# Kernel tuning notes

Measured on AMD Instinct MI355X. Metric: run time of the kernel, lower is better.

## Reference

```python
import jax, jax.numpy as jnp
import numpy as np

B, T, D, S, K = 8, 4096, 1024, 64, 3
EPS = 1e-5

def setup_inputs() -> dict:
    key = jax.random.key(0)
    ks = jax.random.split(key, 10)
    def lin(k, out_d, in_d):
        s = 1.0 / np.sqrt(in_d)
        return jax.random.uniform(k, (out_d, in_d), jnp.float32, -s, s)
    return {
        "x": jax.random.normal(ks[0], (B, T, D), jnp.float32),
        "norm_w": jnp.ones((D,), jnp.float32),
        "norm_b": jnp.zeros((D,), jnp.float32),
        "in_w": lin(ks[1], 2 * D, D),
        "in_b": jnp.zeros((2 * D,), jnp.float32),
        "conv_w": jax.random.normal(ks[2], (D, 1, K), jnp.float32) / np.sqrt(K),
        "conv_b": jnp.zeros((D,), jnp.float32),
        "dt_w": lin(ks[3], S, D),
        "dt_b": jnp.zeros((S,), jnp.float32),
        "b_w": lin(ks[4], S, D),
        "b_b": jnp.zeros((S,), jnp.float32),
        "c_w": lin(ks[5], S, D),
        "c_b": jnp.zeros((S,), jnp.float32),
        "a_log": jax.random.normal(ks[6], (S,), jnp.float32) * 0.02,
        "d": jnp.ones((D,), jnp.float32),
        "out_w": lin(ks[7], D, D + S),
        "out_b": jnp.zeros((D,), jnp.float32),
    }

def reference(x, norm_w, norm_b, in_w, in_b, conv_w, conv_b,
              dt_w, dt_b, b_w, b_b, c_w, c_b, a_log, d, out_w, out_b):
    bsz, tlen, dim = x.shape
    sdim = a_log.shape[0]
    k = conv_w.shape[-1]
    residual = x
    # LayerNorm
    mu = jnp.mean(x, axis=-1, keepdims=True)
    var = jnp.mean(jnp.square(x - mu), axis=-1, keepdims=True)
    xn = (x - mu) * jax.lax.rsqrt(var + EPS) * norm_w + norm_b
    # in_proj and chunk
    h = xn @ in_w.T + in_b                       # (B,T,2D)
    x_proj, z = jnp.split(h, 2, axis=-1)         # each (B,T,D)
    # depthwise conv over time, 'same' padding
    xc = jax.lax.conv_general_dilated(
        x_proj.transpose(0, 2, 1), conv_w, (1,), [(k // 2, k // 2)],
        dimension_numbers=("NCH", "OIH", "NCH"), feature_group_count=dim)
    x_conv = jnp.tanh((xc + conv_b[None, :, None]).transpose(0, 2, 1))  # (B,T,D)
    # gate projections for all timesteps at once
    dt = jax.nn.softplus(z @ dt_w.T + dt_b) + 1e-4   # (B,T,S)
    b = jnp.tanh(z @ b_w.T + b_b)                    # (B,T,S)
    c = jnp.tanh(z @ c_w.T + c_b)                    # (B,T,S)
    a = -jnp.exp(a_log)                              # (S,)
    decay = jnp.exp(a * dt)                          # (B,T,S)
    # linear recurrence: state_t = state_{t-1} * decay_t + b_t
    def step(state, inp):
        dec_t, b_t = inp
        state = state * dec_t + b_t
        return state, state
    _, states = jax.lax.scan(step, jnp.zeros((bsz, sdim), x.dtype),
                             (decay.transpose(1, 0, 2), b.transpose(1, 0, 2)))
    states = states.transpose(1, 0, 2)               # (B,T,S)
    y = c * states
    mix = jnp.concatenate([x_conv * d, y], axis=-1)  # (B,T,D+S)
    out = mix @ out_w.T + out_b                      # (B,T,D)
    return residual + out
```

## Files before the change

kernel.cpp:

```cpp
#include <hip/hip_runtime.h>

#define TT 4096
#define DD 1024
#define NN 32768

typedef short s16x8 __attribute__((ext_vector_type(8)));
typedef float f32x4 __attribute__((ext_vector_type(4)));
typedef unsigned short ushort_t;

__device__ __forceinline__ unsigned short f2bf(float f) {
  unsigned u = __float_as_uint(f);
  u += 0x7FFFu + ((u >> 16) & 1u);
  return (unsigned short)(u >> 16);
}
__device__ __forceinline__ float bf2f(unsigned short h) {
  return __uint_as_float(((unsigned)h) << 16);
}
__device__ __forceinline__ void load_lds16(const void* g, void* l) {
  __builtin_amdgcn_global_load_lds(
      (const __attribute__((address_space(1))) unsigned int*)g,
      (__attribute__((address_space(3))) unsigned int*)l, 16, 0, 0);
}

__global__ __launch_bounds__(256)
void cvt_kernel(const float* __restrict__ s, ushort_t* __restrict__ d, int n) {
  int i = (blockIdx.x * 256 + threadIdx.x) * 4;
  if (i < n) {
    float4 v = *(const float4*)&s[i];
    ushort4 o; o.x = f2bf(v.x); o.y = f2bf(v.y); o.z = f2bf(v.z); o.w = f2bf(v.w);
    *(ushort4*)&d[i] = o;
  }
}

__global__ __launch_bounds__(256)
void w3pad_kernel(const float* __restrict__ dt_w, const float* __restrict__ b_w,
                  const float* __restrict__ c_w, ushort_t* __restrict__ w3) {
  int e = (blockIdx.x * 256 + threadIdx.x) * 4;
  int row = e >> 10, col = e & 1023;
  float4 v; v.x = 0.f; v.y = 0.f; v.z = 0.f; v.w = 0.f;
  if (row < 64)       v = *(const float4*)&dt_w[(row << 10) + col];
  else if (row < 128) v = *(const float4*)&b_w[((row - 64) << 10) + col];
  else if (row < 192) v = *(const float4*)&c_w[((row - 128) << 10) + col];
  ushort4 o; o.x = f2bf(v.x); o.y = f2bf(v.y); o.z = f2bf(v.z); o.w = f2bf(v.w);
  *(ushort4*)&w3[e] = o;
}

__global__ __launch_bounds__(256)
void tpose_kernel(const float* __restrict__ src, ushort_t* __restrict__ dst) {
  __shared__ float tile[64][65];
  int bx = blockIdx.x & 15, by = blockIdx.x >> 4;
  int tx = threadIdx.x & 63, ty0 = threadIdx.x >> 6;
  #pragma unroll
  for (int i = 0; i < 16; ++i) {
    int ty = ty0 * 16 + i;
    tile[ty][tx] = src[(size_t)(by * 64 + ty) * 1024 + bx * 64 + tx];
  }
  __syncthreads();
  #pragma unroll
  for (int i = 0; i < 16; ++i) {
    int ty = ty0 * 16 + i;
    dst[(size_t)(bx * 64 + ty) * 1024 + by * 64 + tx] = f2bf(tile[tx][ty]);
  }
}

__global__ void gbias_kernel(const float* __restrict__ dt_w, const float* __restrict__ b_w,
                             const float* __restrict__ c_w, const float* __restrict__ dt_b,
                             const float* __restrict__ b_b, const float* __restrict__ c_b,
                             const float* __restrict__ in_b, float* __restrict__ gb) {
  int i = blockIdx.x, lane = threadIdx.x;
  const float* wr = i < 64 ? dt_w + (size_t)i * 1024
                  : i < 128 ? b_w + (size_t)(i - 64) * 1024
                            : c_w + (size_t)(i - 128) * 1024;
  float s = 0.f;
  for (int j = lane; j < 1024; j += 64) s += wr[j] * in_b[1024 + j];
  #pragma unroll
  for (int off = 32; off; off >>= 1) s += __shfl_xor(s, off, 64);
  if (lane == 0) {
    float bb = i < 64 ? dt_b[i] : i < 128 ? b_b[i - 64] : c_b[i - 128];
    gb[i] = s + bb;
  }
}

__global__ __launch_bounds__(256)
void ln_kernel(const float* __restrict__ x, const float* __restrict__ w,
               const float* __restrict__ bv, ushort_t* __restrict__ xn)
{
  int row = blockIdx.x * 4 + (threadIdx.x >> 6);
  int lane = threadIdx.x & 63;
  const float* xr = x + (size_t)row * DD;
  float4 v[4];
  float s = 0.f, ss = 0.f;
  #pragma unroll
  for (int j = 0; j < 4; ++j) {
    v[j] = *(const float4*)&xr[j * 256 + lane * 4];
    s  += v[j].x + v[j].y + v[j].z + v[j].w;
    ss += v[j].x * v[j].x + v[j].y * v[j].y + v[j].z * v[j].z + v[j].w * v[j].w;
  }
  #pragma unroll
  for (int off = 32; off > 0; off >>= 1) {
    s  += __shfl_xor(s, off, 64);
    ss += __shfl_xor(ss, off, 64);
  }
  float mean = s * (1.f / 1024.f);
  float var  = ss * (1.f / 1024.f) - mean * mean;
  float rinv = rsqrtf(var + 1e-5f);
  #pragma unroll
  for (int j = 0; j < 4; ++j) {
    int c = j * 256 + lane * 4;
    float4 wv = *(const float4*)&w[c];
    float4 bb = *(const float4*)&bv[c];
    ushort4 o;
    o.x = f2bf((v[j].x - mean) * rinv * wv.x + bb.x);
    o.y = f2bf((v[j].y - mean) * rinv * wv.y + bb.y);
    o.z = f2bf((v[j].z - mean) * rinv * wv.z + bb.z);
    o.w = f2bf((v[j].w - mean) * rinv * wv.w + bb.w);
    *(ushort4*)&xn[(size_t)row * DD + c] = o;
  }
}

template<int EP>
__global__ __launch_bounds__(512, 2)
void gemm256(const ushort_t* __restrict__ A, const ushort_t* __restrict__ W,
             int M, int N, int K,
             const float* __restrict__ bias0,
             ushort_t* __restrict__ o0, ushort_t* __restrict__ o1)
{
  __shared__ ushort_t lds[65536];
  const int tid = threadIdx.x;
  const int lane = tid & 63;
  const int wid = tid >> 6;
  const int wr = wid >> 2;
  const int wc = wid & 3;
  const int lane15 = lane & 15;
  const int lgrp = lane >> 4;
  const int rsw = (lane15 & 7) << 4;
  const int ntn = N >> 8;
  int bid = blockIdx.x;
  { const int cpx = (int)gridDim.x >> 3; bid = (bid & 7) * cpx + (bid >> 3); }
  const int brow = (bid / ntn) << 8;
  const int bcol = (bid % ntn) << 8;
  const int nk = K >> 6;
  const int sRow = tid >> 3;
  const int sCol = (tid & 7) << 4;
  const char* ldsb = (const char*)lds;
  (void)M;

#define STG(bufb, isB, h, kt) do { \
    const int ktc_ = (kt) < nk ? (kt) : nk - 1; \
    const ushort_t* gsrc_ = (isB) ? W : A; \
    const int rowb_ = ((isB) ? bcol : brow) + (h) * 128; \
    _Pragma("unroll") \
    for (int j_ = 0; j_ < 2; ++j_) { \
      const int r_ = j_ * 64 + sRow; \
      load_lds16((const char*)(gsrc_ + (size_t)(rowb_ + r_) * K) + ktc_ * 128 + (sCol ^ ((r_ & 7) << 4)), \
                 (char*)lds + (bufb) * 65536 + (isB) * 32768 + (h) * 16384 + r_ * 128 + sCol); \
    } } while (0)

#define LDA_(bufb, m, kk) \
  (*(const s16x8*)(ldsb + (bufb) * 65536 + wr * 16384 + ((m) * 16 + lane15) * 128 + (((kk) * 64 + lgrp * 16) ^ rsw)))
#define LDB_(bufb, n, kk) \
  (*(const s16x8*)(ldsb + (bufb) * 65536 + 32768 + (wc >> 1) * 16384 + ((wc & 1) * 64 + (n) * 16 + lane15) * 128 + (((kk) * 64 + lgrp * 16) ^ rsw)))

#define BARR() asm volatile("s_barrier" ::: "memory")
#define VMW2() asm volatile("s_waitcnt vmcnt(2)" ::: "memory")
#define VMW4() asm volatile("s_waitcnt vmcnt(4)" ::: "memory")

#define RDA(dst, bufb, mh) do { \
    _Pragma("unroll") for (int kk = 0; kk < 2; ++kk) \
    _Pragma("unroll") for (int q = 0; q < 4; ++q) \
      dst[kk][q] = LDA_(bufb, (mh) * 4 + q, kk); } while (0)
#define RDB(dst, bufb, nh) do { \
    _Pragma("unroll") for (int kk = 0; kk < 2; ++kk) \
    _Pragma("unroll") for (int p = 0; p < 2; ++p) \
      dst[kk][p] = LDB_(bufb, (nh) * 2 + p, kk); } while (0)

#define MFMAQ(AF, BF, mh, nh) do { \
    __builtin_amdgcn_s_setprio(1); \
    _Pragma("unroll") for (int kk = 0; kk < 2; ++kk) \
    _Pragma("unroll") for (int q = 0; q < 4; ++q) \
    _Pragma("unroll") for (int p = 0; p < 2; ++p) \
      acc[(mh) * 4 + q][(nh) * 2 + p] = __builtin_amdgcn_mfma_f32_16x16x32_bf16( \
          AF[kk][q], BF[kk][p], acc[(mh) * 4 + q][(nh) * 2 + p], 0, 0, 0); \
    __builtin_amdgcn_s_setprio(0); } while (0)

  f32x4 acc[8][4];
  #pragma unroll
  for (int m = 0; m < 8; ++m) {
    #pragma unroll
    for (int n = 0; n < 4; ++n) acc[m][n] = (f32x4){0.f, 0.f, 0.f, 0.f};
  }
  s16x8 afP[2][4], afQ[2][4];
  s16x8 b0[2][2], b1[2][2];

  STG(0, 1, 0, 0); STG(0, 0, 0, 0); STG(0, 0, 1, 0); STG(0, 1, 1, 0);
  STG(1, 1, 0, 1); STG(1, 0, 0, 1);
  VMW4(); BARR();
  RDA(afP, 0, 0); RDB(b0, 0, 0);

  const int nIter = nk >> 1;
  for (int it = 0; it < nIter; ++it) {
    const int t0 = 2 * it;
    STG(1, 0, 1, t0 + 1);
    MFMAQ(afP, b0, 0, 0);
    RDB(b1, 0, 1); BARR();
    STG(1, 1, 1, t0 + 1);
    MFMAQ(afP, b1, 0, 1);
    RDA(afQ, 0, 1); BARR();
    STG(0, 1, 0, t0 + 2);
    MFMAQ(afQ, b1, 1, 1);
    VMW2(); BARR();
    STG(0, 0, 0, t0 + 2);
    MFMAQ(afQ, b0, 1, 0);
    RDA(afP, 1, 0); RDB(b1, 1, 1); BARR();
    STG(0, 0, 1, t0 + 2);
    MFMAQ(afP, b1, 0, 1);
    RDB(b0, 1, 0); BARR();
    STG(0, 1, 1, t0 + 2);
    MFMAQ(afP, b0, 0, 0);
    RDA(afQ, 1, 1); BARR();
    STG(1, 1, 0, t0 + 3);
    MFMAQ(afQ, b0, 1, 0);
    VMW2(); BARR();
    STG(1, 0, 0, t0 + 3);
    MFMAQ(afQ, b1, 1, 1);
    RDA(afP, 0, 0); RDB(b0, 0, 0); BARR();
  }
  if (nk & 1) {
    MFMAQ(afP, b0, 0, 0);
    RDB(b1, 0, 1);
    MFMAQ(afP, b1, 0, 1);
    RDA(afQ, 0, 1);
    MFMAQ(afQ, b1, 1, 1);
    MFMAQ(afQ, b0, 1, 0);
  }

#undef STG
#undef LDA_
#undef LDB_
#undef BARR
#undef VMW2
#undef VMW4
#undef RDA
#undef RDB
#undef MFMAQ

  #pragma unroll
  for (int m = 0; m < 8; ++m) {
    #pragma unroll
    for (int i = 0; i < 4; ++i) {
      const int r = brow + wr * 128 + m * 16 + lgrp * 4 + i;
      #pragma unroll
      for (int n = 0; n < 4; ++n) {
        const int col = bcol + wc * 64 + n * 16 + lane15;
        float v = acc[m][n][i] + bias0[col];
        if (col < DD) o0[(size_t)r * DD + col] = f2bf(v);
        else          o1[(size_t)r * DD + (col - DD)] = f2bf(v);
      }
    }
  }
}

__global__ __launch_bounds__(256, 2)
void gemm3_128(const ushort_t* __restrict__ A, const ushort_t* __restrict__ W,
               int M, int N, int K,
               const float* __restrict__ bias, const float* __restrict__ resid,
               float* __restrict__ outf)
{
  __shared__ ushort_t lds[32768];
  const int tid = threadIdx.x;
  const int lane = tid & 63;
  const int wid = tid >> 6;
  const int wr = wid >> 1;
  const int wc = wid & 1;
  const int lane15 = lane & 15;
  const int lgrp = lane >> 4;
  const int rsw = (lane15 & 7) << 4;
  const int ntn = N >> 7;
  int bid = blockIdx.x;
  { const int cpx = (int)gridDim.x >> 3; bid = (bid & 7) * cpx + (bid >> 3); }
  const int brow = (bid / ntn) << 7;
  const int bcol = (bid % ntn) << 7;
  const int nk = K >> 6;
  const int sRow = tid >> 3;
  const int sCol = (tid & 7) << 4;
  const char* ldsb = (const char*)lds;
  (void)M;

  f32x4 acc[4][4];
  #pragma unroll
  for (int q = 0; q < 4; ++q)
    #pragma unroll
    for (int p = 0; p < 4; ++p) acc[q][p] = (f32x4){0.f, 0.f, 0.f, 0.f};

#define STG3(bufb, kt) do { \
    _Pragma("unroll") \
    for (int j_ = 0; j_ < 4; ++j_) { \
      const int r_ = j_ * 32 + sRow; \
      load_lds16((const char*)(A + (size_t)(brow + r_) * K) + (kt) * 128 + (sCol ^ ((r_ & 7) << 4)), \
                 (char*)lds + (bufb) * 32768 + r_ * 128 + sCol); \
      load_lds16((const char*)(W + (size_t)(bcol + r_) * K) + (kt) * 128 + (sCol ^ ((r_ & 7) << 4)), \
                 (char*)lds + (bufb) * 32768 + 16384 + r_ * 128 + sCol); \
    } } while (0)
#define BARR3() asm volatile("s_barrier" ::: "memory")
#define VMW8() asm volatile("s_waitcnt vmcnt(8)" ::: "memory")
#define VMW0() asm volatile("s_waitcnt vmcnt(0)" ::: "memory")

  STG3(0, 0);

  for (int t = 0; t < nk; ++t) {
    const int cur = t & 1;
    if (t + 1 < nk) { STG3(cur ^ 1, t + 1); VMW8(); }
    else            { VMW0(); }
    BARR3();
    #pragma unroll
    for (int kk = 0; kk < 2; ++kk) {
      s16x8 af[4], bf[4];
      #pragma unroll
      for (int q = 0; q < 4; ++q)
        af[q] = *(const s16x8*)(ldsb + cur * 32768 +
                 (wr * 64 + q * 16 + lane15) * 128 + ((kk * 64 + lgrp * 16) ^ rsw));
      #pragma unroll
      for (int p = 0; p < 4; ++p)
        bf[p] = *(const s16x8*)(ldsb + cur * 32768 + 16384 +
                 (wc * 64 + p * 16 + lane15) * 128 + ((kk * 64 + lgrp * 16) ^ rsw));
      __builtin_amdgcn_s_setprio(1);
      #pragma unroll
      for (int q = 0; q < 4; ++q)
        #pragma unroll
        for (int p = 0; p < 4; ++p)
          acc[q][p] = __builtin_amdgcn_mfma_f32_16x16x32_bf16(af[q], bf[p], acc[q][p], 0, 0, 0);
      __builtin_amdgcn_s_setprio(0);
    }
    BARR3();
  }
#undef STG3
#undef BARR3
#undef VMW8
#undef VMW0

  #pragma unroll
  for (int q = 0; q < 4; ++q) {
    #pragma unroll
    for (int i = 0; i < 4; ++i) {
      const int r = brow + wr * 64 + q * 16 + lgrp * 4 + i;
      #pragma unroll
      for (int p = 0; p < 4; ++p) {
        const int col = bcol + wc * 64 + p * 16 + lane15;
        outf[(size_t)r * DD + col] = acc[q][p][i] + bias[col] + resid[(size_t)r * DD + col];
      }
    }
  }
}

__global__ __launch_bounds__(256)
void gemm128w(const ushort_t* __restrict__ A, const ushort_t* __restrict__ W,
              int M, int N, int K, ushort_t* __restrict__ o0)
{
  __shared__ ushort_t As[128 * 64];
  __shared__ ushort_t Bs[128 * 64];
  const int tid = threadIdx.x;
  const int lane = tid & 63;
  const int wid = tid >> 6;
  const int ntn = N >> 7;
  const int brow = (blockIdx.x / ntn) << 7;
  const int bcol = (blockIdx.x % ntn) << 7;
  const int wr = (wid >> 1) << 6;
  const int wc = (wid & 1) << 6;
  const int lane15 = lane & 15;
  const int lgrp = lane >> 4;
  (void)M;

  f32x4 acc[4][4];
  #pragma unroll
  for (int m = 0; m < 4; ++m)
    #pragma unroll
    for (int n = 0; n < 4; ++n)
      acc[m][n] = (f32x4){0.f, 0.f, 0.f, 0.f};

  const int r0 = tid >> 3;
  const int c0 = (tid & 7) << 3;
  const ushort_t* gA = A + (size_t)(brow + r0) * K + c0;
  const ushort_t* gW = W + (size_t)(bcol + r0) * K + c0;
  ushort_t* lA = &As[r0 * 64 + c0];
  ushort_t* lB = &Bs[r0 * 64 + c0];

  for (int k0 = 0; k0 < K; k0 += 64) {
    #pragma unroll
    for (int j = 0; j < 4; ++j) {
      load_lds16(gA + (size_t)(j * 32) * K + k0, lA + j * 32 * 64);
      load_lds16(gW + (size_t)(j * 32) * K + k0, lB + j * 32 * 64);
    }
    __syncthreads();
    #pragma unroll
    for (int kk = 0; kk < 2; ++kk) {
      s16x8 af[4], bfr[4];
      #pragma unroll
      for (int m = 0; m < 4; ++m)
        af[m] = *(const s16x8*)&As[(wr + m * 16 + lane15) * 64 + kk * 32 + lgrp * 8];
      #pragma unroll
      for (int n = 0; n < 4; ++n)
        bfr[n] = *(const s16x8*)&Bs[(wc + n * 16 + lane15) * 64 + kk * 32 + lgrp * 8];
      #pragma unroll
      for (int m = 0; m < 4; ++m)
        #pragma unroll
        for (int n = 0; n < 4; ++n)
          acc[m][n] = __builtin_amdgcn_mfma_f32_16x16x32_bf16(af[m], bfr[n], acc[m][n], 0, 0, 0);
    }
    __syncthreads();
  }

  #pragma unroll
  for (int m = 0; m < 4; ++m) {
    #pragma unroll
    for (int i = 0; i < 4; ++i) {
      const int r = brow + wr + m * 16 + lgrp * 4 + i;
      #pragma unroll
      for (int n = 0; n < 4; ++n) {
        const int col = bcol + wc + n * 16 + lane15;
        o0[(size_t)r * N + col] = f2bf(acc[m][n][i]);
      }
    }
  }
}

__global__ __launch_bounds__(256)
void gemm128g(const ushort_t* __restrict__ A, const ushort_t* __restrict__ W,
              int M, int N, int K,
              const float* __restrict__ gb, const float* __restrict__ alog,
              float* __restrict__ g0, float* __restrict__ g1, float* __restrict__ g2)
{
  __shared__ ushort_t As[128 * 64];
  __shared__ ushort_t Bs[128 * 64];
  const int tid = threadIdx.x;
  const int lane = tid & 63;
  const int wid = tid >> 6;
  const int ntn = N >> 7;
  const int brow = (blockIdx.x / ntn) << 7;
  const int bcol = (blockIdx.x % ntn) << 7;
  const int wr = (wid >> 1) << 6;
  const int wc = (wid & 1) << 6;
  const int lane15 = lane & 15;
  const int lgrp = lane >> 4;
  (void)M;

  f32x4 acc[4][4];
  #pragma unroll
  for (int m = 0; m < 4; ++m)
    #pragma unroll
    for (int n = 0; n < 4; ++n)
      acc[m][n] = (f32x4){0.f, 0.f, 0.f, 0.f};

  const int r0 = tid >> 3;
  const int c0 = (tid & 7) << 3;
  const ushort_t* gA = A + (size_t)(brow + r0) * K + c0;
  const ushort_t* gW = W + (size_t)(bcol + r0) * K + c0;
  ushort_t* lA = &As[r0 * 64 + c0];
  ushort_t* lB = &Bs[r0 * 64 + c0];

  for (int k0 = 0; k0 < K; k0 += 64) {
    #pragma unroll
    for (int j = 0; j < 4; ++j) {
      load_lds16(gA + (size_t)(j * 32) * K + k0, lA + j * 32 * 64);
      load_lds16(gW + (size_t)(j * 32) * K + k0, lB + j * 32 * 64);
    }
    __syncthreads();
    #pragma unroll
    for (int kk = 0; kk < 2; ++kk) {
      s16x8 af[4], bfr[4];
      #pragma unroll
      for (int m = 0; m < 4; ++m)
        af[m] = *(const s16x8*)&As[(wr + m * 16 + lane15) * 64 + kk * 32 + lgrp * 8];
      #pragma unroll
      for (int n = 0; n < 4; ++n)
        bfr[n] = *(const s16x8*)&Bs[(wc + n * 16 + lane15) * 64 + kk * 32 + lgrp * 8];
      #pragma unroll
      for (int m = 0; m < 4; ++m)
        #pragma unroll
        for (int n = 0; n < 4; ++n)
          acc[m][n] = __builtin_amdgcn_mfma_f32_16x16x32_bf16(af[m], bfr[n], acc[m][n], 0, 0, 0);
    }
    __syncthreads();
  }

  #pragma unroll
  for (int m = 0; m < 4; ++m) {
    #pragma unroll
    for (int i = 0; i < 4; ++i) {
      const int r = brow + wr + m * 16 + lgrp * 4 + i;
      #pragma unroll
      for (int n = 0; n < 4; ++n) {
        const int col = bcol + wc + n * 16 + lane15;
        float v = acc[m][n][i];
        if (col < 64) {
          float u = v + gb[col];
          float sp = (u > 20.f) ? u : log1pf(expf(u));
          g0[(size_t)r * 64 + col] = expf(-expf(alog[col]) * (sp + 1e-4f));
        } else if (col < 128) {
          g1[(size_t)r * 64 + (col - 64)] = tanhf(v + gb[col]);
        } else if (col < 192) {
          g2[(size_t)r * 64 + (col - 128)] = tanhf(v + gb[col]);
        }
      }
    }
  }
}

__global__ __launch_bounds__(256)
void conv_kernel(const ushort_t* __restrict__ xp, const float* __restrict__ cw,
                 const float* __restrict__ cb, const float* __restrict__ dvec,
                 ushort_t* __restrict__ mix)
{
  int idx = blockIdx.x * 256 + threadIdx.x;
  int row = idx >> 7;
  int d0 = (idx & 127) << 3;
  int t = row & (TT - 1);
  s16x8 cur = *(const s16x8*)&xp[(size_t)row * DD + d0];
  s16x8 prv; s16x8 nxt;
  #pragma unroll
  for (int j = 0; j < 8; ++j) { prv[j] = 0; nxt[j] = 0; }
  if (t > 0)      prv = *(const s16x8*)&xp[(size_t)(row - 1) * DD + d0];
  if (t < TT - 1) nxt = *(const s16x8*)&xp[(size_t)(row + 1) * DD + d0];
  float wv[24];
  #pragma unroll
  for (int j = 0; j < 6; ++j) *(float4*)&wv[j * 4] = *(const float4*)&cw[d0 * 3 + j * 4];
  float cbv[8], dv[8];
  *(float4*)&cbv[0] = *(const float4*)&cb[d0];
  *(float4*)&cbv[4] = *(const float4*)&cb[d0 + 4];
  *(float4*)&dv[0]  = *(const float4*)&dvec[d0];
  *(float4*)&dv[4]  = *(const float4*)&dvec[d0 + 4];
  s16x8 o;
  #pragma unroll
  for (int j = 0; j < 8; ++j) {
    float acc = cbv[j] + bf2f((ushort_t)prv[j]) * wv[j * 3]
              + bf2f((ushort_t)cur[j]) * wv[j * 3 + 1]
              + bf2f((ushort_t)nxt[j]) * wv[j * 3 + 2];
    o[j] = (short)f2bf(tanhf(acc) * dv[j]);
  }
  *(s16x8*)&mix[(size_t)row * 1088 + d0] = o;
}

__global__ void scanA_kernel(const float* __restrict__ dec, const float* __restrict__ bb,
                             float* __restrict__ P, float* __restrict__ Q)
{
  int b = blockIdx.x >> 6, ci = blockIdx.x & 63, s = threadIdx.x;
  size_t base = (((size_t)b * TT) + ci * 64) * 64 + s;
  float p = 1.f, q = 0.f;
  #pragma unroll 4
  for (int t = 0; t < 64; ++t) {
    float d = dec[base + (size_t)t * 64];
    float w = bb[base + (size_t)t * 64];
    q = q * d + w; p *= d;
  }
  int o = (b * 64 + ci) * 64 + s;
  P[o] = p; Q[o] = q;
}

__global__ void scanB_kernel(const float* __restrict__ P, const float* __restrict__ Q,
                             float* __restrict__ I)
{
  int b = blockIdx.x, s = threadIdx.x;
  float pv[64], qv[64];
  #pragma unroll
  for (int ci = 0; ci < 64; ++ci) {
    int o = (b * 64 + ci) * 64 + s;
    pv[ci] = P[o]; qv[ci] = Q[o];
  }
  float st = 0.f;
  #pragma unroll
  for (int ci = 0; ci < 64; ++ci) {
    int o = (b * 64 + ci) * 64 + s;
    I[o] = st;
    st = st * pv[ci] + qv[ci];
  }
}

__global__ void scanC_kernel(const float* __restrict__ dec, const float* __restrict__ bb,
                             const float* __restrict__ cc, const float* __restrict__ I,
                             ushort_t* __restrict__ mix)
{
  int b = blockIdx.x >> 6, ci = blockIdx.x & 63, s = threadIdx.x;
  size_t base = (((size_t)b * TT) + ci * 64) * 64 + s;
  float st = I[(b * 64 + ci) * 64 + s];
  size_t mrow = (size_t)b * TT + ci * 64;
  #pragma unroll 4
  for (int t = 0; t < 64; ++t) {
    size_t o = base + (size_t)t * 64;
    st = st * dec[o] + bb[o];
    mix[(mrow + t) * 1088 + 1024 + s] = (ushort_t)f2bf(cc[o] * st);
  }
}

extern "C" void kernel_launch(void* const* d_in, const int* in_sizes, int n_in,
                              void* d_out, int out_size, void* d_ws, size_t ws_size,
                              hipStream_t stream)
{
  (void)in_sizes; (void)n_in; (void)out_size; (void)ws_size;
  const float* x      = (const float*)d_in[0];
  const float* norm_w = (const float*)d_in[1];
  const float* norm_b = (const float*)d_in[2];
  const float* in_w   = (const float*)d_in[3];
  const float* in_b   = (const float*)d_in[4];
  const float* conv_w = (const float*)d_in[5];
  const float* conv_b = (const float*)d_in[6];
  const float* dt_w   = (const float*)d_in[7];
  const float* dt_b   = (const float*)d_in[8];
  const float* b_w    = (const float*)d_in[9];
  const float* b_b    = (const float*)d_in[10];
  const float* c_w    = (const float*)d_in[11];
  const float* c_b    = (const float*)d_in[12];
  const float* a_log  = (const float*)d_in[13];
  const float* dvec   = (const float*)d_in[14];
  const float* out_w  = (const float*)d_in[15];
  const float* out_b  = (const float*)d_in[16];
  float* out = (float*)d_out;

  char* p = (char*)d_ws;
  ushort_t* mix    = (ushort_t*)p;
  ushort_t* xn     = mix;
  p += 71303168;
  ushort_t* xproj  = (ushort_t*)p; p += 67108864;
  char*     zreg   = p;            p += 67108864;
  ushort_t* w1_bf  = (ushort_t*)p; p += 4194304;
  ushort_t* w3     = (ushort_t*)p; p += 524288;
  ushort_t* outw_bf= (ushort_t*)p; p += 2228224;
  float* P = (float*)p; p += 131072;
  float* Q = (float*)p; p += 131072;
  float* I = (float*)p; p += 131072;

  float* gdec = (float*)zreg;
  float* gbb  = (float*)(zreg + 8388608);
  float* gcc  = (float*)(zreg + 16777216);
  ushort_t* inw2t  = (ushort_t*)(zreg + 33554432);
  float*    gb     = (float*)(zreg + 37748736);
  ushort_t* wgates = (ushort_t*)(zreg + 41943040);

  cvt_kernel<<<1024, 256, 0, stream>>>(in_w, w1_bf, 1048576);
  cvt_kernel<<<1088, 256, 0, stream>>>(out_w, outw_bf, 1114112);
  tpose_kernel<<<256, 256, 0, stream>>>(in_w + 1048576, inw2t);
  w3pad_kernel<<<256, 256, 0, stream>>>(dt_w, b_w, c_w, w3);
  gemm128w<<<16, 256, 0, stream>>>(w3, inw2t, 256, 1024, 1024, wgates);
  gbias_kernel<<<192, 64, 0, stream>>>(dt_w, b_w, c_w, dt_b, b_b, c_b, in_b, gb);

  ln_kernel<<<8192, 256, 0, stream>>>(x, norm_w, norm_b, xn);

  gemm256<0><<<(NN / 256) * (1024 / 256), 512, 0, stream>>>(
      xn, w1_bf, NN, 1024, 1024, in_b, xproj, nullptr);

  gemm128g<<<(NN / 128) * (256 / 128), 256, 0, stream>>>(
      xn, wgates, NN, 256, 1024, gb, a_log, gdec, gbb, gcc);

  conv_kernel<<<NN * 128 / 256, 256, 0, stream>>>(xproj, conv_w, conv_b, dvec, mix);

  scanA_kernel<<<512, 64, 0, stream>>>(gdec, gbb, P, Q);
  scanB_kernel<<<8, 64, 0, stream>>>(P, Q, I);
  scanC_kernel<<<512, 64, 0, stream>>>(gdec, gbb, gcc, I, mix);

  gemm3_128<<<(NN / 128) * (1024 / 128), 256, 0, stream>>>(
      mix, outw_bf, NN, 1024, 1088, out_b, x, out);
}
```

Measured before the change: 393.2 us.

## Merge prep kernels, fuse conv with scanC, widen output GEMM tile to 128x256

Folds the four weight-conversion and transpose kernels into one launch, and the gate-weight GEMM plus gate-bias reduction into a second. The depthwise conv and the final scan pass become one launch by splitting on block index. The output GEMM moves to 512-thread blocks with a 128x256 tile, so the activation tile is reused across more columns. The aim is fewer launches and less A-tile reloading, at the cost of one block per CU and a larger LDS footprint.

```diff
diff --git a/kernel.cpp b/kernel.cpp
--- a/kernel.cpp
+++ b/kernel.cpp
@@ -23,61 +23,142 @@
 }
 
 __global__ __launch_bounds__(256)
-void cvt_kernel(const float* __restrict__ s, ushort_t* __restrict__ d, int n) {
-  int i = (blockIdx.x * 256 + threadIdx.x) * 4;
-  if (i < n) {
-    float4 v = *(const float4*)&s[i];
+void prep1_kernel(const float* __restrict__ in_w, const float* __restrict__ out_w,
+                  const float* __restrict__ dt_w, const float* __restrict__ b_w,
+                  const float* __restrict__ c_w,
+                  ushort_t* __restrict__ w1_bf, ushort_t* __restrict__ outw_bf,
+                  ushort_t* __restrict__ w3, ushort_t* __restrict__ inw2t)
+{
+  __shared__ float tile[64][65];
+  int blk = blockIdx.x, tid = threadIdx.x;
+  if (blk < 1024) {
+    int i = (blk * 256 + tid) * 4;
+    float4 v = *(const float4*)&in_w[i];
     ushort4 o; o.x = f2bf(v.x); o.y = f2bf(v.y); o.z = f2bf(v.z); o.w = f2bf(v.w);
-    *(ushort4*)&d[i] = o;
+    *(ushort4*)&w1_bf[i] = o;
+  } else if (blk < 2112) {
+    int i = ((blk - 1024) * 256 + tid) * 4;
+    if (i < 1114112) {
+      float4 v = *(const float4*)&out_w[i];
+      ushort4 o; o.x = f2bf(v.x); o.y = f2bf(v.y); o.z = f2bf(v.z); o.w = f2bf(v.w);
+      *(ushort4*)&outw_bf[i] = o;
+    }
+  } else if (blk < 2368) {
+    int e = ((blk - 2112) * 256 + tid) * 4;
+    int row = e >> 10, col = e & 1023;
+    float4 v; v.x = 0.f; v.y = 0.f; v.z = 0.f; v.w = 0.f;
+    if (row < 64)       v = *(const float4*)&dt_w[(row << 10) + col];
+    else if (row < 128) v = *(const float4*)&b_w[((row - 64) << 10) + col];
+    else if (row < 192) v = *(const float4*)&c_w[((row - 128) << 10) + col];
+    ushort4 o; o.x = f2bf(v.x); o.y = f2bf(v.y); o.z = f2bf(v.z); o.w = f2bf(v.w);
+    *(ushort4*)&w3[e] = o;
+  } else {
+    int b2 = blk - 2368;
+    int bx = b2 & 15, by = b2 >> 4;
+    int tx = tid & 63, ty0 = tid >> 6;
+    const float* src = in_w + 1048576;
+    #pragma unroll
+    for (int i = 0; i < 16; ++i) {
+      int ty = ty0 * 16 + i;
+      tile[ty][tx] = src[(size_t)(by * 64 + ty) * 1024 + bx * 64 + tx];
+    }
+    __syncthreads();
+    #pragma unroll
+    for (int i = 0; i < 16; ++i) {
+      int ty = ty0 * 16 + i;
+      inw2t[(size_t)(bx * 64 + ty) * 1024 + by * 64 + tx] = f2bf(tile[tx][ty]);
+    }
   }
 }
 
 __global__ __launch_bounds__(256)
-void w3pad_kernel(const float* __restrict__ dt_w, const float* __restrict__ b_w,
-                  const float* __restrict__ c_w, ushort_t* __restrict__ w3) {
-  int e = (blockIdx.x * 256 + threadIdx.x) * 4;
-  int row = e >> 10, col = e & 1023;
-  float4 v; v.x = 0.f; v.y = 0.f; v.z = 0.f; v.w = 0.f;
-  if (row < 64)       v = *(const float4*)&dt_w[(row << 10) + col];
-  else if (row < 128) v = *(const float4*)&b_w[((row - 64) << 10) + col];
-  else if (row < 192) v = *(const float4*)&c_w[((row - 128) << 10) + col];
-  ushort4 o; o.x = f2bf(v.x); o.y = f2bf(v.y); o.z = f2bf(v.z); o.w = f2bf(v.w);
-  *(ushort4*)&w3[e] = o;
-}
-
-__global__ __launch_bounds__(256)
-void tpose_kernel(const float* __restrict__ src, ushort_t* __restrict__ dst) {
-  __shared__ float tile[64][65];
-  int bx = blockIdx.x & 15, by = blockIdx.x >> 4;
-  int tx = threadIdx.x & 63, ty0 = threadIdx.x >> 6;
-  #pragma unroll
-  for (int i = 0; i < 16; ++i) {
-    int ty = ty0 * 16 + i;
-    tile[ty][tx] = src[(size_t)(by * 64 + ty) * 1024 + bx * 64 + tx];
-  }
-  __syncthreads();
-  #pragma unroll
-  for (int i = 0; i < 16; ++i) {
-    int ty = ty0 * 16 + i;
-    dst[(size_t)(bx * 64 + ty) * 1024 + by * 64 + tx] = f2bf(tile[tx][ty]);
-  }
-}
-
-__global__ void gbias_kernel(const float* __restrict__ dt_w, const float* __restrict__ b_w,
-                             const float* __restrict__ c_w, const float* __restrict__ dt_b,
-                             const float* __restrict__ b_b, const float* __restrict__ c_b,
-                             const float* __restrict__ in_b, float* __restrict__ gb) {
-  int i = blockIdx.x, lane = threadIdx.x;
-  const float* wr = i < 64 ? dt_w + (size_t)i * 1024
-                  : i < 128 ? b_w + (size_t)(i - 64) * 1024
-                            : c_w + (size_t)(i - 128) * 1024;
-  float s = 0.f;
-  for (int j = lane; j < 1024; j += 64) s += wr[j] * in_b[1024 + j];
-  #pragma unroll
-  for (int off = 32; off; off >>= 1) s += __shfl_xor(s, off, 64);
-  if (lane == 0) {
-    float bb = i < 64 ? dt_b[i] : i < 128 ? b_b[i - 64] : c_b[i - 128];
-    gb[i] = s + bb;
+void prep2_kernel(const ushort_t* __restrict__ w3, const ushort_t* __restrict__ inw2t,
+                  ushort_t* __restrict__ wgates,
+                  const float* __restrict__ dt_w, const float* __restrict__ b_w,
+                  const float* __restrict__ c_w, const float* __restrict__ dt_b,
+                  const float* __restrict__ b_b, const float* __restrict__ c_b,
+                  const float* __restrict__ in_b, float* __restrict__ gb)
+{
+  __shared__ ushort_t As[128 * 64];
+  __shared__ ushort_t Bs[128 * 64];
+  const int tid = threadIdx.x;
+  if (blockIdx.x >= 16) {
+    int i = (blockIdx.x - 16) * 4 + (tid >> 6);
+    int lane = tid & 63;
+    const float* wr = i < 64 ? dt_w + (size_t)i * 1024
+                    : i < 128 ? b_w + (size_t)(i - 64) * 1024
+                              : c_w + (size_t)(i - 128) * 1024;
+    float s = 0.f;
+    for (int j = lane; j < 1024; j += 64) s += wr[j] * in_b[1024 + j];
+    #pragma unroll
+    for (int off = 32; off; off >>= 1) s += __shfl_xor(s, off, 64);
+    if (lane == 0) {
+      float bb = i < 64 ? dt_b[i] : i < 128 ? b_b[i - 64] : c_b[i - 128];
+      gb[i] = s + bb;
+    }
+    return;
+  }
+  const int K = 1024, N = 1024;
+  const int bid = blockIdx.x;
+  const int lane = tid & 63;
+  const int wid = tid >> 6;
+  const int brow = (bid / 8) << 7;
+  const int bcol = (bid % 8) << 7;
+  const int wr = (wid >> 1) << 6;
+  const int wc = (wid & 1) << 6;
+  const int lane15 = lane & 15;
+  const int lgrp = lane >> 4;
+
+  f32x4 acc[4][4];
+  #pragma unroll
+  for (int m = 0; m < 4; ++m)
+    #pragma unroll
+    for (int n = 0; n < 4; ++n)
+      acc[m][n] = (f32x4){0.f, 0.f, 0.f, 0.f};
+
+  const int r0 = tid >> 3;
+  const int c0 = (tid & 7) << 3;
+  const ushort_t* gA = w3 + (size_t)(brow + r0) * K + c0;
+  const ushort_t* gW = inw2t + (size_t)(bcol + r0) * K + c0;
+  ushort_t* lA = &As[r0 * 64 + c0];
+  ushort_t* lB = &Bs[r0 * 64 + c0];
+
+  for (int k0 = 0; k0 < K; k0 += 64) {
+    #pragma unroll
+    for (int j = 0; j < 4; ++j) {
+      load_lds16(gA + (size_t)(j * 32) * K + k0, lA + j * 32 * 64);
+      load_lds16(gW + (size_t)(j * 32) * K + k0, lB + j * 32 * 64);
+    }
+    __syncthreads();
+    #pragma unroll
+    for (int kk = 0; kk < 2; ++kk) {
+      s16x8 af[4], bfr[4];
+      #pragma unroll
+      for (int m = 0; m < 4; ++m)
+        af[m] = *(const s16x8*)&As[(wr + m * 16 + lane15) * 64 + kk * 32 + lgrp * 8];
+      #pragma unroll
+      for (int n = 0; n < 4; ++n)
+        bfr[n] = *(const s16x8*)&Bs[(wc + n * 16 + lane15) * 64 + kk * 32 + lgrp * 8];
+      #pragma unroll
+      for (int m = 0; m < 4; ++m)
+        #pragma unroll
+        for (int n = 0; n < 4; ++n)
+          acc[m][n] = __builtin_amdgcn_mfma_f32_16x16x32_bf16(af[m], bfr[n], acc[m][n], 0, 0, 0);
+    }
+    __syncthreads();
+  }
+
+  #pragma unroll
+  for (int m = 0; m < 4; ++m) {
+    #pragma unroll
+    for (int i = 0; i < 4; ++i) {
+      const int r = brow + wr + m * 16 + lgrp * 4 + i;
+      #pragma unroll
+      for (int n = 0; n < 4; ++n) {
+        const int col = bcol + wc + n * 16 + lane15;
+        wgates[(size_t)r * N + col] = f2bf(acc[m][n][i]);
+      }
+    }
   }
 }
 
@@ -260,26 +341,26 @@
   }
 }
 
-__global__ __launch_bounds__(256, 2)
-void gemm3_128(const ushort_t* __restrict__ A, const ushort_t* __restrict__ W,
-               int M, int N, int K,
-               const float* __restrict__ bias, const float* __restrict__ resid,
-               float* __restrict__ outf)
-{
-  __shared__ ushort_t lds[32768];
+__global__ __launch_bounds__(512, 1)
+void gemm3_v2(const ushort_t* __restrict__ A, const ushort_t* __restrict__ W,
+              int M, int N, int K,
+              const float* __restrict__ bias, const float* __restrict__ resid,
+              float* __restrict__ outf)
+{
+  __shared__ ushort_t lds[49152];
   const int tid = threadIdx.x;
   const int lane = tid & 63;
   const int wid = tid >> 6;
-  const int wr = wid >> 1;
-  const int wc = wid & 1;
+  const int wr2 = wid >> 2;
+  const int wc4 = wid & 3;
   const int lane15 = lane & 15;
   const int lgrp = lane >> 4;
   const int rsw = (lane15 & 7) << 4;
-  const int ntn = N >> 7;
+  const int ntn = N >> 8;
   int bid = blockIdx.x;
   { const int cpx = (int)gridDim.x >> 3; bid = (bid & 7) * cpx + (bid >> 3); }
   const int brow = (bid / ntn) << 7;
-  const int bcol = (bid % ntn) << 7;
+  const int bcol = (bid % ntn) << 8;
   const int nk = K >> 6;
   const int sRow = tid >> 3;
   const int sCol = (tid & 7) << 4;
@@ -294,22 +375,26 @@
 
 #define STG3(bufb, kt) do { \
     _Pragma("unroll") \
+    for (int j_ = 0; j_ < 2; ++j_) { \
+      const int r_ = j_ * 64 + sRow; \
+      load_lds16((const char*)(A + (size_t)(brow + r_) * K) + (kt) * 128 + (sCol ^ ((r_ & 7) << 4)), \
+                 (char*)lds + (bufb) * 49152 + r_ * 128 + sCol); \
+    } \
+    _Pragma("unroll") \
     for (int j_ = 0; j_ < 4; ++j_) { \
-      const int r_ = j_ * 32 + sRow; \
-      load_lds16((const char*)(A + (size_t)(brow + r_) * K) + (kt) * 128 + (sCol ^ ((r_ & 7) << 4)), \
-                 (char*)lds + (bufb) * 32768 + r_ * 128 + sCol); \
+      const int r_ = j_ * 64 + sRow; \
       load_lds16((const char*)(W + (size_t)(bcol + r_) * K) + (kt) * 128 + (sCol ^ ((r_ & 7) << 4)), \
-                 (char*)lds + (bufb) * 32768 + 16384 + r_ * 128 + sCol); \
+                 (char*)lds + (bufb) * 49152 + 16384 + r_ * 128 + sCol); \
     } } while (0)
 #define BARR3() asm volatile("s_barrier" ::: "memory")
-#define VMW8() asm volatile("s_waitcnt vmcnt(8)" ::: "memory")
+#define VMW6() asm volatile("s_waitcnt vmcnt(6)" ::: "memory")
 #define VMW0() asm volatile("s_waitcnt vmcnt(0)" ::: "memory")
 
   STG3(0, 0);
 
   for (int t = 0; t < nk; ++t) {
     const int cur = t & 1;
-    if (t + 1 < nk) { STG3(cur ^ 1, t + 1); VMW8(); }
+    if (t + 1 < nk) { STG3(cur ^ 1, t + 1); VMW6(); }
     else            { VMW0(); }
     BARR3();
     #pragma unroll
@@ -317,12 +402,12 @@
       s16x8 af[4], bf[4];
       #pragma unroll
       for (int q = 0; q < 4; ++q)
-        af[q] = *(const s16x8*)(ldsb + cur * 32768 +
-                 (wr * 64 + q * 16 + lane15) * 128 + ((kk * 64 + lgrp * 16) ^ rsw));
+        af[q] = *(const s16x8*)(ldsb + cur * 49152 +
+                 (wr2 * 64 + q * 16 + lane15) * 128 + ((kk * 64 + lgrp * 16) ^ rsw));
       #pragma unroll
       for (int p = 0; p < 4; ++p)
-        bf[p] = *(const s16x8*)(ldsb + cur * 32768 + 16384 +
-                 (wc * 64 + p * 16 + lane15) * 128 + ((kk * 64 + lgrp * 16) ^ rsw));
+        bf[p] = *(const s16x8*)(ldsb + cur * 49152 + 16384 +
+                 (wc4 * 64 + p * 16 + lane15) * 128 + ((kk * 64 + lgrp * 16) ^ rsw));
       __builtin_amdgcn_s_setprio(1);
       #pragma unroll
       for (int q = 0; q < 4; ++q)
@@ -335,17 +420,17 @@
   }
 #undef STG3
 #undef BARR3
-#undef VMW8
+#undef VMW6
 #undef VMW0
 
   #pragma unroll
   for (int q = 0; q < 4; ++q) {
     #pragma unroll
     for (int i = 0; i < 4; ++i) {
-      const int r = brow + wr * 64 + q * 16 + lgrp * 4 + i;
+      const int r = brow + wr2 * 64 + q * 16 + lgrp * 4 + i;
       #pragma unroll
       for (int p = 0; p < 4; ++p) {
-        const int col = bcol + wc * 64 + p * 16 + lane15;
+        const int col = bcol + wc4 * 64 + p * 16 + lane15;
         outf[(size_t)r * DD + col] = acc[q][p][i] + bias[col] + resid[(size_t)r * DD + col];
       }
     }
@@ -353,8 +438,10 @@
 }
 
 __global__ __launch_bounds__(256)
-void gemm128w(const ushort_t* __restrict__ A, const ushort_t* __restrict__ W,
-              int M, int N, int K, ushort_t* __restrict__ o0)
+void gemm128g(const ushort_t* __restrict__ A, const ushort_t* __restrict__ W,
+              int M, int N, int K,
+              const float* __restrict__ gb, const float* __restrict__ alog,
+              float* __restrict__ g0, float* __restrict__ g1, float* __restrict__ g2)
 {
   __shared__ ushort_t As[128 * 64];
   __shared__ ushort_t Bs[128 * 64];
@@ -417,79 +504,6 @@
       #pragma unroll
       for (int n = 0; n < 4; ++n) {
         const int col = bcol + wc + n * 16 + lane15;
-        o0[(size_t)r * N + col] = f2bf(acc[m][n][i]);
-      }
-    }
-  }
-}
-
-__global__ __launch_bounds__(256)
-void gemm128g(const ushort_t* __restrict__ A, const ushort_t* __restrict__ W,
-              int M, int N, int K,
-              const float* __restrict__ gb, const float* __restrict__ alog,
-              float* __restrict__ g0, float* __restrict__ g1, float* __restrict__ g2)
-{
-  __shared__ ushort_t As[128 * 64];
-  __shared__ ushort_t Bs[128 * 64];
-  const int tid = threadIdx.x;
-  const int lane = tid & 63;
-  const int wid = tid >> 6;
-  const int ntn = N >> 7;
-  const int brow = (blockIdx.x / ntn) << 7;
-  const int bcol = (blockIdx.x % ntn) << 7;
-  const int wr = (wid >> 1) << 6;
-  const int wc = (wid & 1) << 6;
-  const int lane15 = lane & 15;
-  const int lgrp = lane >> 4;
-  (void)M;
-
-  f32x4 acc[4][4];
-  #pragma unroll
-  for (int m = 0; m < 4; ++m)
-    #pragma unroll
-    for (int n = 0; n < 4; ++n)
-      acc[m][n] = (f32x4){0.f, 0.f, 0.f, 0.f};
-
-  const int r0 = tid >> 3;
-  const int c0 = (tid & 7) << 3;
-  const ushort_t* gA = A + (size_t)(brow + r0) * K + c0;
-  const ushort_t* gW = W + (size_t)(bcol + r0) * K + c0;
-  ushort_t* lA = &As[r0 * 64 + c0];
-  ushort_t* lB = &Bs[r0 * 64 + c0];
-
-  for (int k0 = 0; k0 < K; k0 += 64) {
-    #pragma unroll
-    for (int j = 0; j < 4; ++j) {
-      load_lds16(gA + (size_t)(j * 32) * K + k0, lA + j * 32 * 64);
-      load_lds16(gW + (size_t)(j * 32) * K + k0, lB + j * 32 * 64);
-    }
-    __syncthreads();
-    #pragma unroll
-    for (int kk = 0; kk < 2; ++kk) {
-      s16x8 af[4], bfr[4];
-      #pragma unroll
-      for (int m = 0; m < 4; ++m)
-        af[m] = *(const s16x8*)&As[(wr + m * 16 + lane15) * 64 + kk * 32 + lgrp * 8];
-      #pragma unroll
-      for (int n = 0; n < 4; ++n)
-        bfr[n] = *(const s16x8*)&Bs[(wc + n * 16 + lane15) * 64 + kk * 32 + lgrp * 8];
-      #pragma unroll
-      for (int m = 0; m < 4; ++m)
-        #pragma unroll
-        for (int n = 0; n < 4; ++n)
-          acc[m][n] = __builtin_amdgcn_mfma_f32_16x16x32_bf16(af[m], bfr[n], acc[m][n], 0, 0, 0);
-    }
-    __syncthreads();
-  }
-
-  #pragma unroll
-  for (int m = 0; m < 4; ++m) {
-    #pragma unroll
-    for (int i = 0; i < 4; ++i) {
-      const int r = brow + wr + m * 16 + lgrp * 4 + i;
-      #pragma unroll
-      for (int n = 0; n < 4; ++n) {
-        const int col = bcol + wc + n * 16 + lane15;
         float v = acc[m][n][i];
         if (col < 64) {
           float u = v + gb[col];
@@ -506,37 +520,53 @@
 }
 
 __global__ __launch_bounds__(256)
-void conv_kernel(const ushort_t* __restrict__ xp, const float* __restrict__ cw,
-                 const float* __restrict__ cb, const float* __restrict__ dvec,
-                 ushort_t* __restrict__ mix)
-{
-  int idx = blockIdx.x * 256 + threadIdx.x;
-  int row = idx >> 7;
-  int d0 = (idx & 127) << 3;
-  int t = row & (TT - 1);
-  s16x8 cur = *(const s16x8*)&xp[(size_t)row * DD + d0];
-  s16x8 prv; s16x8 nxt;
-  #pragma unroll
-  for (int j = 0; j < 8; ++j) { prv[j] = 0; nxt[j] = 0; }
-  if (t > 0)      prv = *(const s16x8*)&xp[(size_t)(row - 1) * DD + d0];
-  if (t < TT - 1) nxt = *(const s16x8*)&xp[(size_t)(row + 1) * DD + d0];
-  float wv[24];
-  #pragma unroll
-  for (int j = 0; j < 6; ++j) *(float4*)&wv[j * 4] = *(const float4*)&cw[d0 * 3 + j * 4];
-  float cbv[8], dv[8];
-  *(float4*)&cbv[0] = *(const float4*)&cb[d0];
-  *(float4*)&cbv[4] = *(const float4*)&cb[d0 + 4];
-  *(float4*)&dv[0]  = *(const float4*)&dvec[d0];
-  *(float4*)&dv[4]  = *(const float4*)&dvec[d0 + 4];
-  s16x8 o;
-  #pragma unroll
-  for (int j = 0; j < 8; ++j) {
-    float acc = cbv[j] + bf2f((ushort_t)prv[j]) * wv[j * 3]
-              + bf2f((ushort_t)cur[j]) * wv[j * 3 + 1]
-              + bf2f((ushort_t)nxt[j]) * wv[j * 3 + 2];
-    o[j] = (short)f2bf(tanhf(acc) * dv[j]);
-  }
-  *(s16x8*)&mix[(size_t)row * 1088 + d0] = o;
+void convscanC_kernel(const ushort_t* __restrict__ xp, const float* __restrict__ cw,
+                      const float* __restrict__ cb, const float* __restrict__ dvec,
+                      const float* __restrict__ dec, const float* __restrict__ bb,
+                      const float* __restrict__ cc, const float* __restrict__ I,
+                      ushort_t* __restrict__ mix)
+{
+  if (blockIdx.x < 16384) {
+    int idx = blockIdx.x * 256 + threadIdx.x;
+    int row = idx >> 7;
+    int d0 = (idx & 127) << 3;
+    int t = row & (TT - 1);
+    s16x8 cur = *(const s16x8*)&xp[(size_t)row * DD + d0];
+    s16x8 prv; s16x8 nxt;
+    #pragma unroll
+    for (int j = 0; j < 8; ++j) { prv[j] = 0; nxt[j] = 0; }
+    if (t > 0)      prv = *(const s16x8*)&xp[(size_t)(row - 1) * DD + d0];
+    if (t < TT - 1) nxt = *(const s16x8*)&xp[(size_t)(row + 1) * DD + d0];
+    float wv[24];
+    #pragma unroll
+    for (int j = 0; j < 6; ++j) *(float4*)&wv[j * 4] = *(const float4*)&cw[d0 * 3 + j * 4];
+    float cbv[8], dv[8];
+    *(float4*)&cbv[0] = *(const float4*)&cb[d0];
+    *(float4*)&cbv[4] = *(const float4*)&cb[d0 + 4];
+    *(float4*)&dv[0]  = *(const float4*)&dvec[d0];
+    *(float4*)&dv[4]  = *(const float4*)&dvec[d0 + 4];
+    s16x8 o;
+    #pragma unroll
+    for (int j = 0; j < 8; ++j) {
+      float acc = cbv[j] + bf2f((ushort_t)prv[j]) * wv[j * 3]
+                + bf2f((ushort_t)cur[j]) * wv[j * 3 + 1]
+                + bf2f((ushort_t)nxt[j]) * wv[j * 3 + 2];
+      o[j] = (short)f2bf(tanhf(acc) * dv[j]);
+    }
+    *(s16x8*)&mix[(size_t)row * 1088 + d0] = o;
+  } else {
+    int unit = (blockIdx.x - 16384) * 4 + (threadIdx.x >> 6);
+    int b = unit >> 6, ci = unit & 63, s = threadIdx.x & 63;
+    size_t base = (((size_t)b * TT) + ci * 64) * 64 + s;
+    float st = I[(b * 64 + ci) * 64 + s];
+    size_t mrow = (size_t)b * TT + ci * 64;
+    #pragma unroll 4
+    for (int t = 0; t < 64; ++t) {
+      size_t o = base + (size_t)t * 64;
+      st = st * dec[o] + bb[o];
+      mix[(mrow + t) * 1088 + 1024 + s] = (ushort_t)f2bf(cc[o] * st);
+    }
+  }
 }
 
 __global__ void scanA_kernel(const float* __restrict__ dec, const float* __restrict__ bb,
@@ -571,22 +601,6 @@
     int o = (b * 64 + ci) * 64 + s;
     I[o] = st;
     st = st * pv[ci] + qv[ci];
-  }
-}
-
-__global__ void scanC_kernel(const float* __restrict__ dec, const float* __restrict__ bb,
-                             const float* __restrict__ cc, const float* __restrict__ I,
-                             ushort_t* __restrict__ mix)
-{
-  int b = blockIdx.x >> 6, ci = blockIdx.x & 63, s = threadIdx.x;
-  size_t base = (((size_t)b * TT) + ci * 64) * 64 + s;
-  float st = I[(b * 64 + ci) * 64 + s];
-  size_t mrow = (size_t)b * TT + ci * 64;
-  #pragma unroll 4
-  for (int t = 0; t < 64; ++t) {
-    size_t o = base + (size_t)t * 64;
-    st = st * dec[o] + bb[o];
-    mix[(mrow + t) * 1088 + 1024 + s] = (ushort_t)f2bf(cc[o] * st);
   }
 }
 
@@ -634,12 +648,10 @@
   float*    gb     = (float*)(zreg + 37748736);
   ushort_t* wgates = (ushort_t*)(zreg + 41943040);
 
-  cvt_kernel<<<1024, 256, 0, stream>>>(in_w, w1_bf, 1048576);
-  cvt_kernel<<<1088, 256, 0, stream>>>(out_w, outw_bf, 1114112);
-  tpose_kernel<<<256, 256, 0, stream>>>(in_w + 1048576, inw2t);
-  w3pad_kernel<<<256, 256, 0, stream>>>(dt_w, b_w, c_w, w3);
-  gemm128w<<<16, 256, 0, stream>>>(w3, inw2t, 256, 1024, 1024, wgates);
-  gbias_kernel<<<192, 64, 0, stream>>>(dt_w, b_w, c_w, dt_b, b_b, c_b, in_b, gb);
+  prep1_kernel<<<2624, 256, 0, stream>>>(in_w, out_w, dt_w, b_w, c_w,
+                                         w1_bf, outw_bf, w3, inw2t);
+  prep2_kernel<<<64, 256, 0, stream>>>(w3, inw2t, wgates,
+                                       dt_w, b_w, c_w, dt_b, b_b, c_b, in_b, gb);
 
   ln_kernel<<<8192, 256, 0, stream>>>(x, norm_w, norm_b, xn);
 
@@ -649,12 +661,12 @@
   gemm128g<<<(NN / 128) * (256 / 128), 256, 0, stream>>>(
       xn, wgates, NN, 256, 1024, gb, a_log, gdec, gbb, gcc);
 
-  conv_kernel<<<NN * 128 / 256, 256, 0, stream>>>(xproj, conv_w, conv_b, dvec, mix);
-
   scanA_kernel<<<512, 64, 0, stream>>>(gdec, gbb, P, Q);
   scanB_kernel<<<8, 64, 0, stream>>>(P, Q, I);
-  scanC_kernel<<<512, 64, 0, stream>>>(gdec, gbb, gcc, I, mix);
-
-  gemm3_128<<<(NN / 128) * (1024 / 128), 256, 0, stream>>>(
+
+  convscanC_kernel<<<16512, 256, 0, stream>>>(xproj, conv_w, conv_b, dvec,
+                                              gdec, gbb, gcc, I, mix);
+
+  gemm3_v2<<<(NN / 128) * (1024 / 256), 512, 0, stream>>>(
       mix, outw_bf, NN, 1024, 1088, out_b, x, out);
 }
```

Result: no change. 386.4 us (-1.7%).
